# Kernel tuning notes

Measured on AMD Instinct MI355X. Metric: run time of the kernel, lower is better.

The kernel has to match this reference:

```python
import jax, jax.numpy as jnp
import numpy as np

N_EMBD = 1024
N_HEAD = 16
HEAD_DIM = N_EMBD // N_HEAD


def setup_inputs() -> dict:
    key = jax.random.key(0)
    kx, kq, kk, kv, ko = jax.random.split(key, 5)
    s = 1.0 / np.sqrt(N_EMBD)
    return {
        "x": jax.random.normal(kx, (4, 2048, N_EMBD), dtype=jnp.float32),
        "Wq": jax.random.normal(kq, (N_EMBD, N_EMBD), dtype=jnp.float32) * s,
        "Wk": jax.random.normal(kk, (N_EMBD, N_EMBD), dtype=jnp.float32) * s,
        "Wv": jax.random.normal(kv, (N_EMBD, N_EMBD), dtype=jnp.float32) * s,
        "Wo": jax.random.normal(ko, (N_EMBD, N_EMBD), dtype=jnp.float32) * s,
    }


def reference(x, Wq, Wk, Wv, Wo):
    B, T, C = x.shape
    H, D = N_HEAD, HEAD_DIM
    # projections; torch Linear computes x @ W.T
    q = (x @ Wq.T).reshape(B, T, H, D).transpose(0, 2, 1, 3)  # [B,H,T,D]
    k = (x @ Wk.T).reshape(B, T, H, D).transpose(0, 2, 1, 3)
    v = (x @ Wv.T).reshape(B, T, H, D).transpose(0, 2, 1, 3)
    scores = jnp.einsum("bhtd,bhsd->bhts", q, k) / np.sqrt(D).astype(np.float32)
    causal = jnp.tril(jnp.ones((T, T), dtype=bool))
    scores = jnp.where(causal, scores, -jnp.inf)
    attn = jax.nn.softmax(scores, axis=-1)
    out = jnp.einsum("bhts,bhsd->bhtd", attn, v)  # [B,H,T,D]
    out = out.transpose(0, 2, 1, 3).reshape(B, T, C)
    return out @ Wo.T
```

## Files before the change

kernel.cpp:

```cpp
#include <hip/hip_runtime.h>
#include <hip/hip_bf16.h>


typedef __bf16 bf16_t;
typedef __bf16 bf16x4 __attribute__((ext_vector_type(4)));
typedef __bf16 bf16x8 __attribute__((ext_vector_type(8)));
typedef float  f32x4  __attribute__((ext_vector_type(4)));

#define MFMA16(a, b, c) __builtin_amdgcn_mfma_f32_16x16x32_bf16(a, b, c, 0, 0, 0)

__device__ __forceinline__ float exp2_(float x) {
#if __has_builtin(__builtin_amdgcn_exp2f)
    return __builtin_amdgcn_exp2f(x);
#else
    return __expf(x * 0.6931471805599453f);
#endif
}

__device__ __forceinline__ void gload_lds16(const bf16_t* g, bf16_t* l) {
    __builtin_amdgcn_global_load_lds(
        (const __attribute__((address_space(1))) void*)g,
        (__attribute__((address_space(3))) void*)l, 16, 0, 0);
}

__global__ __launch_bounds__(256)
void cast_all(const float* __restrict__ x,  const float* __restrict__ Wq,
              const float* __restrict__ Wk, const float* __restrict__ Wv,
              const float* __restrict__ Wo,
              bf16_t* __restrict__ xb, bf16_t* __restrict__ wqkv,
              bf16_t* __restrict__ wob) {
    int i = blockIdx.x * 256 + threadIdx.x;
    const float* src;
    bf16_t* dst;
    if (blockIdx.y == 0) {
        src = x; dst = xb;
    } else {
        if (i >= 524288) return;
        int wsel = i >> 17;
        int loc  = i & 131071;
        src = wsel == 0 ? Wq : wsel == 1 ? Wk : wsel == 2 ? Wv : Wo;
        dst = wsel == 3 ? wob : wqkv + (size_t)wsel * 1048576;
        i = loc;
    }
    const float4* p = (const float4*)src;
    float4 a = p[i * 2], b = p[i * 2 + 1];
    bf16x8 o;
    o[0] = (bf16_t)a.x; o[1] = (bf16_t)a.y; o[2] = (bf16_t)a.z; o[3] = (bf16_t)a.w;
    o[4] = (bf16_t)b.x; o[5] = (bf16_t)b.y; o[6] = (bf16_t)b.z; o[7] = (bf16_t)b.w;
    *(bf16x8*)(dst + (size_t)i * 8) = o;
}

template<int OUT_BF16>
__global__ __launch_bounds__(512, 2)
void gemm_8ph(const bf16_t* __restrict__ A, const bf16_t* __restrict__ B,
              void* __restrict__ Cv, int M, int N, int K) {
    __shared__ bf16_t sm[2][24576];
    const int tid = threadIdx.x;
    const int lane = tid & 63, w = tid >> 6;
    const int wr = w >> 1, wc = w & 1;
    const int g = lane >> 4, c = lane & 15;
    const long bm = (long)blockIdx.x * 256;
    const long bn = (long)blockIdx.y * 128;

    const int srow8 = tid >> 3;
    const int pb = tid & 7;

    auto STAGE_A = [&](int buf, int h, int kt) {
        #pragma unroll
        for (int r = 0; r < 2; ++r) {
            int row = h * 128 + r * 64 + srow8;
            int lb  = pb ^ (row & 7);
            gload_lds16(A + (bm + row) * (long)K + kt * 64 + lb * 8,
                        &sm[buf][row * 64 + pb * 8]);
        }
    };
    auto STAGE_B = [&](int buf, int kt) {
        #pragma unroll
        for (int r = 0; r < 2; ++r) {
            int row = r * 64 + srow8;
            int lb  = pb ^ (row & 7);
            gload_lds16(B + (bn + row) * (long)K + kt * 64 + lb * 8,
                        &sm[buf][16384 + row * 64 + pb * 8]);
        }
    };
    auto LDA = [&](int buf, int m, int k) -> bf16x8 {
        int row = wr * 64 + m * 16 + c;
        return *(const bf16x8*)&sm[buf][row * 64 + (((k * 4 + g) ^ (row & 7)) * 8)];
    };
    auto LDB = [&](int buf, int n, int k) -> bf16x8 {
        int row = wc * 64 + n * 16 + c;
        return *(const bf16x8*)&sm[buf][16384 + row * 64 +
                                        (((k * 4 + g) ^ (row & 7)) * 8)];
    };

#define PHASE(BUF, MM, ISSUE_STMT, WAIT_STMT)                          \
    {                                                                  \
        bf16x8 a0 = LDA(BUF, MM, 0), a1 = LDA(BUF, MM, 1);             \
        ISSUE_STMT;                                                    \
        WAIT_STMT;                                                     \
        __builtin_amdgcn_s_barrier();                                  \
        asm volatile("s_waitcnt lgkmcnt(0)" ::: "memory");             \
        __builtin_amdgcn_sched_barrier(0);                             \
        __builtin_amdgcn_s_setprio(1);                                 \
        _Pragma("unroll")                                              \
        for (int n = 0; n < 4; ++n) {                                  \
            acc[MM][n] = MFMA16(a0, bfr[n][0], acc[MM][n]);            \
            acc[MM][n] = MFMA16(a1, bfr[n][1], acc[MM][n]);            \
        }                                                              \
        __builtin_amdgcn_s_setprio(0);                                 \
        __builtin_amdgcn_s_barrier();                                  \
    }

    f32x4 acc[4][4] = {};
    bf16x8 bfr[4][2];
    const int NJ = K / 128;

    STAGE_B(0, 0); STAGE_A(0, 0, 0); STAGE_A(0, 1, 0);
    STAGE_B(1, 1);
    asm volatile("s_waitcnt vmcnt(2)" ::: "memory");
    __builtin_amdgcn_s_barrier();

    for (int j = 0; j < NJ; ++j) {
        const int t0 = 2 * j;
        const bool more = (j + 1 < NJ);

        #pragma unroll
        for (int n = 0; n < 4; ++n) { bfr[n][0] = LDB(0, n, 0); bfr[n][1] = LDB(0, n, 1); }
        PHASE(0, 0, STAGE_A(1, 0, t0 + 1), (void)0);
        PHASE(0, 1, STAGE_A(1, 1, t0 + 1), (void)0);
        PHASE(0, 2, if (more) STAGE_B(0, t0 + 2), (void)0);
        PHASE(0, 3, (void)0,
              if (more) { asm volatile("s_waitcnt vmcnt(2)" ::: "memory"); }
              else      { asm volatile("s_waitcnt vmcnt(0)" ::: "memory"); });

        #pragma unroll
        for (int n = 0; n < 4; ++n) { bfr[n][0] = LDB(1, n, 0); bfr[n][1] = LDB(1, n, 1); }
        PHASE(1, 0, if (more) STAGE_A(0, 0, t0 + 2), (void)0);
        PHASE(1, 1, if (more) STAGE_A(0, 1, t0 + 2), (void)0);
        PHASE(1, 2, if (more) STAGE_B(1, t0 + 3), (void)0);
        PHASE(1, 3, (void)0,
              if (more) { asm volatile("s_waitcnt vmcnt(2)" ::: "memory"); });
    }
#undef PHASE

    #pragma unroll
    for (int m = 0; m < 4; ++m)
        #pragma unroll
        for (int n = 0; n < 4; ++n)
            #pragma unroll
            for (int i = 0; i < 4; ++i) {
                long row = bm + wr * 64 + m * 16 + g * 4 + i;
                long col = bn + wc * 64 + n * 16 + c;
                float v = acc[m][n][i];
                if (OUT_BF16) ((bf16_t*)Cv)[row * N + col] = (bf16_t)v;
                else          ((float*)Cv)[row * N + col]  = v;
            }
}


__device__ __forceinline__ void stage_K(const bf16_t* Kp, long rowb, int kb, int hcol,
                                        bf16_t* Kbuf, int tid) {
    int row = tid >> 3;
    int lb  = (tid & 7) ^ (row & 7);
    gload_lds16(Kp + (rowb + kb + row) * 3072 + hcol + lb * 8, Kbuf + tid * 8);
}

__device__ __forceinline__ bf16x8 load_V8(const bf16_t* Vp, long rowb, int kb,
                                          int hcol, int tid) {
    const int d  = tid & 63;
    const int k0 = (tid >> 6) * 8;
    bf16x8 v;
    #pragma unroll
    for (int j = 0; j < 8; ++j)
        v[j] = Vp[(rowb + kb + k0 + j) * 3072 + hcol + d];
    return v;
}

__device__ __forceinline__ void write_V8(bf16_t* Vbuf, int tid, bf16x8 v) {
    const int d  = tid & 63;
    const int k0 = (tid >> 6) * 8;
    *(bf16x8*)&Vbuf[d * 72 + k0] = v;
}

__global__ __launch_bounds__(512, 6)
void attn_kernel(const bf16_t* __restrict__ Qp, const bf16_t* __restrict__ Kp,
                 const bf16_t* __restrict__ Vp, bf16_t* __restrict__ O) {
    __shared__ bf16_t Ks[2][64 * 64];
    __shared__ bf16_t Vts[2][64 * 72];
    __shared__ bf16_t PW[8][16 * 72];

    const int tid = threadIdx.x, lane = tid & 63, w = tid >> 6;
    const int g = lane >> 4, c = lane & 15;
    const int bh = blockIdx.x;
    const int b = bh >> 4, h = bh & 15;
    const long rowb = (long)b * 2048;
    const int hcol = h * 64;
    const float QSCL = 0.18033688011112042f;

    const int q0  = 15 - blockIdx.y;
    const int qlo = q0 * 128 + w * 16;
    const int nkt = 2 * q0 + 2;

    bf16x8 qf[2];
    #pragma unroll
    for (int ks = 0; ks < 2; ++ks) {
        qf[ks] = *(const bf16x8*)(Qp + (rowb + qlo + c) * 3072 +
                                  hcol + ks * 32 + g * 8);
        #pragma unroll
        for (int j = 0; j < 8; ++j)
            qf[ks][j] = (bf16_t)((float)qf[ks][j] * QSCL);
    }

    float m_r = -1e30f;
    float l_r = 0.f;
    f32x4 acc[4] = {};

    stage_K(Kp, rowb, 0, hcol, Ks[0], tid);
    write_V8(Vts[0], tid, load_V8(Vp, rowb, 0, hcol, tid));
    __syncthreads();

    for (int t = 0; t < nkt; ++t) {
        const int cur = t & 1;
        const int kb = t * 64;
        const bool pre = (t + 1 < nkt);
        bf16x8 vreg;
        if (pre) {
            stage_K(Kp, rowb, kb + 64, hcol, Ks[cur ^ 1], tid);
            vreg = load_V8(Vp, rowb, kb + 64, hcol, tid);
        }

        if (kb <= qlo + 15) {
            f32x4 sacc[4] = {};
            __builtin_amdgcn_s_setprio(1);
            #pragma unroll
            for (int nt = 0; nt < 4; ++nt) {
                const int row = nt * 16 + c;
                #pragma unroll
                for (int ks = 0; ks < 2; ++ks) {
                    bf16x8 kf = *(const bf16x8*)&Ks[cur][row * 64 +
                                    (((ks * 4 + g) ^ (c & 7)) * 8)];
                    sacc[nt] = MFMA16(kf, qf[ks], sacc[nt]);
                }
            }
            __builtin_amdgcn_s_setprio(0);
            if (kb + 63 > qlo) {
                const int q = qlo + c;
                #pragma unroll
                for (int nt = 0; nt < 4; ++nt)
                    #pragma unroll
                    for (int i = 0; i < 4; ++i) {
                        int key = kb + nt * 16 + g * 4 + i;
                        if (key > q) sacc[nt][i] = -1e30f;
                    }
            }

            float m0 = fmaxf(fmaxf(sacc[0][0], sacc[0][1]),
                             fmaxf(fmaxf(sacc[0][2], sacc[0][3]), sacc[1][0]));
            float m1 = fmaxf(fmaxf(sacc[1][1], sacc[1][2]),
                             fmaxf(fmaxf(sacc[1][3], sacc[2][0]), sacc[2][1]));
            float m2 = fmaxf(fmaxf(sacc[2][2], sacc[2][3]),
                             fmaxf(fmaxf(sacc[3][0], sacc[3][1]),
                                   fmaxf(sacc[3][2], sacc[3][3])));
            float mx = fmaxf(fmaxf(m0, m1), m2);
            if (__any(mx > m_r + 8.f)) {
                mx = fmaxf(mx, __shfl_xor(mx, 16, 64));
                mx = fmaxf(mx, __shfl_xor(mx, 32, 64));
                float mnew = fmaxf(m_r, mx);
                float scl = exp2_(m_r - mnew);
                #pragma unroll
                for (int nt = 0; nt < 4; ++nt)
                    acc[nt] *= scl;
                l_r *= scl;
                m_r = mnew;
            }
            float rsn[4];
            #pragma unroll
            for (int nt = 0; nt < 4; ++nt) {
                #pragma unroll
                for (int i = 0; i < 4; ++i)
                    sacc[nt][i] = exp2_(sacc[nt][i] - m_r);
                rsn[nt] = (sacc[nt][0] + sacc[nt][1]) + (sacc[nt][2] + sacc[nt][3]);
            }
            l_r += (rsn[0] + rsn[1]) + (rsn[2] + rsn[3]);

            #pragma unroll
            for (int nt = 0; nt < 4; ++nt) {
                bf16x4 t4;
                #pragma unroll
                for (int i = 0; i < 4; ++i) t4[i] = (bf16_t)sacc[nt][i];
                *(bf16x4*)&PW[w][c * 72 + nt * 16 + g * 4] = t4;
            }

            __builtin_amdgcn_s_setprio(1);
            #pragma unroll
            for (int ks = 0; ks < 2; ++ks) {
                bf16x8 pf = *(const bf16x8*)&PW[w][c * 72 + ks * 32 + g * 8];
                #pragma unroll
                for (int nt = 0; nt < 4; ++nt) {
                    bf16x8 vf = *(const bf16x8*)&Vts[cur][(nt * 16 + c) * 72 +
                                                          ks * 32 + g * 8];
                    acc[nt] = MFMA16(vf, pf, acc[nt]);
                }
            }
            __builtin_amdgcn_s_setprio(0);
        }

        if (pre) write_V8(Vts[cur ^ 1], tid, vreg);
        __syncthreads();
    }

    l_r += __shfl_xor(l_r, 16, 64);
    l_r += __shfl_xor(l_r, 32, 64);
    {
        float rl = __builtin_amdgcn_rcpf(l_r);
        #pragma unroll
        for (int nt = 0; nt < 4; ++nt) {
            bf16x4 t4;
            #pragma unroll
            for (int i = 0; i < 4; ++i) t4[i] = (bf16_t)(acc[nt][i] * rl);
            *(bf16x4*)&PW[w][c * 72 + nt * 16 + g * 4] = t4;
        }
    }
    #pragma unroll
    for (int p = 0; p < 2; ++p) {
        int row = p * 8 + (lane >> 3);
        int ch  = (lane & 7) * 8;
        bf16x8 v = *(const bf16x8*)&PW[w][row * 72 + ch];
        *(bf16x8*)&O[(rowb + qlo + row) * 1024 + hcol + ch] = v;
    }
}

extern "C" void kernel_launch(void* const* d_in, const int* in_sizes, int n_in,
                              void* d_out, int out_size, void* d_ws, size_t ws_size,
                              hipStream_t stream) {
    const float* x  = (const float*)d_in[0];
    const float* Wq = (const float*)d_in[1];
    const float* Wk = (const float*)d_in[2];
    const float* Wv = (const float*)d_in[3];
    const float* Wo = (const float*)d_in[4];

    const int M = 8192;
    const int C = 1024;

    char* ws = (char*)d_ws;
    bf16_t* xb   = (bf16_t*)(ws);
    bf16_t* wqkv = (bf16_t*)(ws + ((size_t)16 << 20));
    bf16_t* wob  = (bf16_t*)(ws + ((size_t)22 << 20));
    bf16_t* qkv  = (bf16_t*)(ws + ((size_t)24 << 20));
    bf16_t* aob  = (bf16_t*)(ws + ((size_t)72 << 20));

    cast_all<<<dim3(4096, 2), 256, 0, stream>>>(x, Wq, Wk, Wv, Wo, xb, wqkv, wob);

    gemm_8ph<1><<<dim3(M / 256, 3072 / 128), 512, 0, stream>>>(xb, wqkv, qkv, M, 3072, C);

    attn_kernel<<<dim3(64, 16), 512, 0, stream>>>(
        qkv, qkv + 1024, qkv + 2048, aob);

    gemm_8ph<0><<<dim3(M / 256, C / 128), 512, 0, stream>>>(aob, wob, d_out, M, C, C);
}
```

Before: 159.8 us.

## Double attention query tile per wave and swizzle V/P LDS layouts

Each wave now handles 32 query rows (two 16-row MFMA tiles) instead of 16, so a block covers 256 queries and every K/V fragment read from LDS feeds two MFMAs. The grid in y halves and the causal-tile ordering is remapped. The V transpose buffer and the P scratch drop their padding and use XOR swizzles to avoid bank conflicts while shrinking LDS. The trade-off is higher register pressure from doubled accumulators and coarser causal work per block, which may hurt occupancy and load balance.

```diff
diff --git a/kernel.cpp b/kernel.cpp
--- a/kernel.cpp
+++ b/kernel.cpp
@@ -178,16 +178,16 @@
 
 __device__ __forceinline__ void write_V8(bf16_t* Vbuf, int tid, bf16x8 v) {
     const int d  = tid & 63;
-    const int k0 = (tid >> 6) * 8;
-    *(bf16x8*)&Vbuf[d * 72 + k0] = v;
+    const int ch = (tid >> 6) ^ (d & 7);
+    *(bf16x8*)&Vbuf[d * 64 + ch * 8] = v;
 }
 
 __global__ __launch_bounds__(512, 6)
 void attn_kernel(const bf16_t* __restrict__ Qp, const bf16_t* __restrict__ Kp,
                  const bf16_t* __restrict__ Vp, bf16_t* __restrict__ O) {
     __shared__ bf16_t Ks[2][64 * 64];
-    __shared__ bf16_t Vts[2][64 * 72];
-    __shared__ bf16_t PW[8][16 * 72];
+    __shared__ bf16_t Vts[2][64 * 64];
+    __shared__ bf16_t PW[8][32 * 32];
 
     const int tid = threadIdx.x, lane = tid & 63, w = tid >> 6;
     const int g = lane >> 4, c = lane & 15;
@@ -197,23 +197,26 @@
     const int hcol = h * 64;
     const float QSCL = 0.18033688011112042f;
 
-    const int q0  = 15 - blockIdx.y;
-    const int qlo = q0 * 128 + w * 16;
-    const int nkt = 2 * q0 + 2;
-
-    bf16x8 qf[2];
+    const int by = blockIdx.y;
+    const int q0 = by < 4 ? 7 - by : by - 4;
+    const int qlo = q0 * 256 + w * 32;
+    const int nkt = 4 * q0 + 4;
+
+    bf16x8 qf[2][2];
     #pragma unroll
-    for (int ks = 0; ks < 2; ++ks) {
-        qf[ks] = *(const bf16x8*)(Qp + (rowb + qlo + c) * 3072 +
-                                  hcol + ks * 32 + g * 8);
-        #pragma unroll
-        for (int j = 0; j < 8; ++j)
-            qf[ks][j] = (bf16_t)((float)qf[ks][j] * QSCL);
-    }
-
-    float m_r = -1e30f;
-    float l_r = 0.f;
-    f32x4 acc[4] = {};
+    for (int m = 0; m < 2; ++m)
+        #pragma unroll
+        for (int ks = 0; ks < 2; ++ks) {
+            qf[m][ks] = *(const bf16x8*)(Qp + (rowb + qlo + m * 16 + c) * 3072 +
+                                         hcol + ks * 32 + g * 8);
+            #pragma unroll
+            for (int j = 0; j < 8; ++j)
+                qf[m][ks][j] = (bf16_t)((float)qf[m][ks][j] * QSCL);
+        }
+
+    float m_r[2] = {-1e30f, -1e30f};
+    float l_r[2] = {0.f, 0.f};
+    f32x4 acc[2][4] = {};
 
     stage_K(Kp, rowb, 0, hcol, Ks[0], tid);
     write_V8(Vts[0], tid, load_V8(Vp, rowb, 0, hcol, tid));
@@ -229,8 +232,8 @@
             vreg = load_V8(Vp, rowb, kb + 64, hcol, tid);
         }
 
-        if (kb <= qlo + 15) {
-            f32x4 sacc[4] = {};
+        if (kb <= qlo + 31) {
+            f32x4 sacc[2][4] = {};
             __builtin_amdgcn_s_setprio(1);
             #pragma unroll
             for (int nt = 0; nt < 4; ++nt) {
@@ -238,95 +241,133 @@
                 #pragma unroll
                 for (int ks = 0; ks < 2; ++ks) {
                     bf16x8 kf = *(const bf16x8*)&Ks[cur][row * 64 +
-                                    (((ks * 4 + g) ^ (c & 7)) * 8)];
-                    sacc[nt] = MFMA16(kf, qf[ks], sacc[nt]);
+                                    (((ks * 4 + g) ^ (row & 7)) * 8)];
+                    sacc[0][nt] = MFMA16(kf, qf[0][ks], sacc[0][nt]);
+                    sacc[1][nt] = MFMA16(kf, qf[1][ks], sacc[1][nt]);
                 }
             }
             __builtin_amdgcn_s_setprio(0);
             if (kb + 63 > qlo) {
-                const int q = qlo + c;
-                #pragma unroll
-                for (int nt = 0; nt < 4; ++nt)
+                #pragma unroll
+                for (int m = 0; m < 2; ++m) {
+                    const int q = qlo + m * 16 + c;
                     #pragma unroll
-                    for (int i = 0; i < 4; ++i) {
-                        int key = kb + nt * 16 + g * 4 + i;
-                        if (key > q) sacc[nt][i] = -1e30f;
+                    for (int nt = 0; nt < 4; ++nt)
+                        #pragma unroll
+                        for (int i = 0; i < 4; ++i) {
+                            int key = kb + nt * 16 + g * 4 + i;
+                            if (key > q) sacc[m][nt][i] = -1e30f;
+                        }
+                }
+            }
+
+            float mx[2];
+            #pragma unroll
+            for (int m = 0; m < 2; ++m) {
+                float a0 = fmaxf(fmaxf(sacc[m][0][0], sacc[m][0][1]),
+                                 fmaxf(fmaxf(sacc[m][0][2], sacc[m][0][3]), sacc[m][1][0]));
+                float a1 = fmaxf(fmaxf(sacc[m][1][1], sacc[m][1][2]),
+                                 fmaxf(fmaxf(sacc[m][1][3], sacc[m][2][0]), sacc[m][2][1]));
+                float a2 = fmaxf(fmaxf(sacc[m][2][2], sacc[m][2][3]),
+                                 fmaxf(fmaxf(sacc[m][3][0], sacc[m][3][1]),
+                                       fmaxf(sacc[m][3][2], sacc[m][3][3])));
+                mx[m] = fmaxf(fmaxf(a0, a1), a2);
+            }
+            if (__any(fmaxf(mx[0] - m_r[0], mx[1] - m_r[1]) > 8.f)) {
+                #pragma unroll
+                for (int m = 0; m < 2; ++m) {
+                    float mm = mx[m];
+                    mm = fmaxf(mm, __shfl_xor(mm, 16, 64));
+                    mm = fmaxf(mm, __shfl_xor(mm, 32, 64));
+                    float mnew = fmaxf(m_r[m], mm);
+                    float scl = exp2_(m_r[m] - mnew);
+                    #pragma unroll
+                    for (int nt = 0; nt < 4; ++nt)
+                        acc[m][nt] *= scl;
+                    l_r[m] *= scl;
+                    m_r[m] = mnew;
+                }
+            }
+            #pragma unroll
+            for (int m = 0; m < 2; ++m) {
+                float rsn[4];
+                #pragma unroll
+                for (int nt = 0; nt < 4; ++nt) {
+                    #pragma unroll
+                    for (int i = 0; i < 4; ++i)
+                        sacc[m][nt][i] = exp2_(sacc[m][nt][i] - m_r[m]);
+                    rsn[nt] = (sacc[m][nt][0] + sacc[m][nt][1]) +
+                              (sacc[m][nt][2] + sacc[m][nt][3]);
+                }
+                l_r[m] += (rsn[0] + rsn[1]) + (rsn[2] + rsn[3]);
+            }
+
+            #pragma unroll
+            for (int ks = 0; ks < 2; ++ks) {
+                #pragma unroll
+                for (int m = 0; m < 2; ++m)
+                    #pragma unroll
+                    for (int n2 = 0; n2 < 2; ++n2) {
+                        int nt = 2 * ks + n2;
+                        bf16x4 t4;
+                        #pragma unroll
+                        for (int i = 0; i < 4; ++i) t4[i] = (bf16_t)sacc[m][nt][i];
+                        int u = n2 * 4 + g;
+                        *(bf16x4*)&PW[w][(m * 16 + c) * 32 + ((u ^ (c & 7)) * 4)] = t4;
                     }
-            }
-
-            float m0 = fmaxf(fmaxf(sacc[0][0], sacc[0][1]),
-                             fmaxf(fmaxf(sacc[0][2], sacc[0][3]), sacc[1][0]));
-            float m1 = fmaxf(fmaxf(sacc[1][1], sacc[1][2]),
-                             fmaxf(fmaxf(sacc[1][3], sacc[2][0]), sacc[2][1]));
-            float m2 = fmaxf(fmaxf(sacc[2][2], sacc[2][3]),
-                             fmaxf(fmaxf(sacc[3][0], sacc[3][1]),
-                                   fmaxf(sacc[3][2], sacc[3][3])));
-            float mx = fmaxf(fmaxf(m0, m1), m2);
-            if (__any(mx > m_r + 8.f)) {
-                mx = fmaxf(mx, __shfl_xor(mx, 16, 64));
-                mx = fmaxf(mx, __shfl_xor(mx, 32, 64));
-                float mnew = fmaxf(m_r, mx);
-                float scl = exp2_(m_r - mnew);
-                #pragma unroll
-                for (int nt = 0; nt < 4; ++nt)
-                    acc[nt] *= scl;
-                l_r *= scl;
-                m_r = mnew;
-            }
-            float rsn[4];
-            #pragma unroll
-            for (int nt = 0; nt < 4; ++nt) {
-                #pragma unroll
-                for (int i = 0; i < 4; ++i)
-                    sacc[nt][i] = exp2_(sacc[nt][i] - m_r);
-                rsn[nt] = (sacc[nt][0] + sacc[nt][1]) + (sacc[nt][2] + sacc[nt][3]);
-            }
-            l_r += (rsn[0] + rsn[1]) + (rsn[2] + rsn[3]);
-
-            #pragma unroll
-            for (int nt = 0; nt < 4; ++nt) {
-                bf16x4 t4;
-                #pragma unroll
-                for (int i = 0; i < 4; ++i) t4[i] = (bf16_t)sacc[nt][i];
-                *(bf16x4*)&PW[w][c * 72 + nt * 16 + g * 4] = t4;
-            }
-
-            __builtin_amdgcn_s_setprio(1);
-            #pragma unroll
-            for (int ks = 0; ks < 2; ++ks) {
-                bf16x8 pf = *(const bf16x8*)&PW[w][c * 72 + ks * 32 + g * 8];
-                #pragma unroll
-                for (int nt = 0; nt < 4; ++nt) {
-                    bf16x8 vf = *(const bf16x8*)&Vts[cur][(nt * 16 + c) * 72 +
-                                                          ks * 32 + g * 8];
-                    acc[nt] = MFMA16(vf, pf, acc[nt]);
+                __builtin_amdgcn_s_setprio(1);
+                #pragma unroll
+                for (int m = 0; m < 2; ++m) {
+                    int prow = (m * 16 + c) * 32;
+                    bf16x4 plo = *(const bf16x4*)&PW[w][prow + (((2 * g)     ^ (c & 7)) * 4)];
+                    bf16x4 phi = *(const bf16x4*)&PW[w][prow + (((2 * g + 1) ^ (c & 7)) * 4)];
+                    union { struct { bf16x4 lo, hi; } p; bf16x8 v; } cb;
+                    cb.p.lo = plo; cb.p.hi = phi;
+                    #pragma unroll
+                    for (int nt = 0; nt < 4; ++nt) {
+                        const int row = nt * 16 + c;
+                        bf16x8 vf = *(const bf16x8*)&Vts[cur][row * 64 +
+                                        (((ks * 4 + g) ^ (row & 7)) * 8)];
+                        acc[m][nt] = MFMA16(vf, cb.v, acc[m][nt]);
+                    }
                 }
-            }
-            __builtin_amdgcn_s_setprio(0);
+                __builtin_amdgcn_s_setprio(0);
+            }
         }
 
         if (pre) write_V8(Vts[cur ^ 1], tid, vreg);
         __syncthreads();
     }
 
-    l_r += __shfl_xor(l_r, 16, 64);
-    l_r += __shfl_xor(l_r, 32, 64);
-    {
-        float rl = __builtin_amdgcn_rcpf(l_r);
-        #pragma unroll
-        for (int nt = 0; nt < 4; ++nt) {
-            bf16x4 t4;
-            #pragma unroll
-            for (int i = 0; i < 4; ++i) t4[i] = (bf16_t)(acc[nt][i] * rl);
-            *(bf16x4*)&PW[w][c * 72 + nt * 16 + g * 4] = t4;
-        }
-    }
     #pragma unroll
-    for (int p = 0; p < 2; ++p) {
-        int row = p * 8 + (lane >> 3);
-        int ch  = (lane & 7) * 8;
-        bf16x8 v = *(const bf16x8*)&PW[w][row * 72 + ch];
-        *(bf16x8*)&O[(rowb + qlo + row) * 1024 + hcol + ch] = v;
+    for (int m = 0; m < 2; ++m) {
+        l_r[m] += __shfl_xor(l_r[m], 16, 64);
+        l_r[m] += __shfl_xor(l_r[m], 32, 64);
+    }
+    #pragma unroll
+    for (int m = 0; m < 2; ++m) {
+        float rl = __builtin_amdgcn_rcpf(l_r[m]);
+        #pragma unroll
+        for (int hh = 0; hh < 2; ++hh) {
+            #pragma unroll
+            for (int n2 = 0; n2 < 2; ++n2) {
+                int nt = 2 * hh + n2;
+                bf16x4 t4;
+                #pragma unroll
+                for (int i = 0; i < 4; ++i) t4[i] = (bf16_t)(acc[m][nt][i] * rl);
+                int u = n2 * 4 + g;
+                *(bf16x4*)&PW[w][(m * 16 + c) * 32 + ((u ^ (c & 7)) * 4)] = t4;
+            }
+            int row16 = lane >> 2;
+            int ub = (lane & 3) * 2;
+            int prow = (m * 16 + row16) * 32;
+            bf16x4 e0 = *(const bf16x4*)&PW[w][prow + ((ub       ^ (row16 & 7)) * 4)];
+            bf16x4 e1 = *(const bf16x4*)&PW[w][prow + (((ub + 1) ^ (row16 & 7)) * 4)];
+            union { struct { bf16x4 lo, hi; } p; bf16x8 v; } cb;
+            cb.p.lo = e0; cb.p.hi = e1;
+            *(bf16x8*)&O[(rowb + qlo + m * 16 + row16) * 1024 +
+                         hcol + hh * 32 + (lane & 3) * 8] = cb.v;
+        }
     }
 }
 
@@ -353,7 +394,7 @@
 
     gemm_8ph<1><<<dim3(M / 256, 3072 / 128), 512, 0, stream>>>(xb, wqkv, qkv, M, 3072, C);
 
-    attn_kernel<<<dim3(64, 16), 512, 0, stream>>>(
+    attn_kernel<<<dim3(64, 8), 512, 0, stream>>>(
         qkv, qkv + 1024, qkv + 2048, aob);
 
     gemm_8ph<0><<<dim3(M / 256, C / 128), 512, 0, stream>>>(aob, wob, d_out, M, C, C);
```

Result: slower. 399.2 us (+149.7%).
